# Optimization experiments

Measured on AMD Instinct MI355X. Metric: run time of the kernel, lower is better.

## Reference

```python
import jax, jax.numpy as jnp
import numpy as np

B, V, E, D_IN, D_OUT = 8, 10000, 160000, 128, 128
BN_EPS = 1e-5


def setup_inputs() -> dict:
    key = jax.random.key(0)
    ks = jax.random.split(key, 8)
    X = jax.random.normal(ks[0], (B, V, D_IN), dtype=jnp.float32)
    edge_attr = jax.random.normal(ks[1], (B, E), dtype=jnp.float32)
    W_node = jax.random.normal(ks[2], (D_OUT, D_IN), dtype=jnp.float32) * (1.0 / np.sqrt(D_IN))
    W_edge = jax.random.normal(ks[3], (D_OUT, 1), dtype=jnp.float32)
    W_self = jax.random.normal(ks[4], (D_OUT, D_IN), dtype=jnp.float32) * (1.0 / np.sqrt(D_IN))
    b_self = jax.random.normal(ks[5], (D_OUT,), dtype=jnp.float32) * 0.01
    gamma = jnp.ones((D_OUT,), dtype=jnp.float32)
    beta = jnp.zeros((D_OUT,), dtype=jnp.float32)
    edge_index = jax.random.randint(ks[6], (E, 2), 0, V, dtype=jnp.int32)
    return {"X": X, "edge_attr": edge_attr, "W_node": W_node, "W_edge": W_edge,
            "W_self": W_self, "b_self": b_self, "gamma": gamma, "beta": beta,
            "edge_index": edge_index}


def reference(X, edge_attr, W_node, W_edge, W_self, b_self, gamma, beta, edge_index):
    src = edge_index[:, 0]  # [E]
    dst = edge_index[:, 1]  # [E]
    # self-loop linear
    H = jnp.einsum('bvf,of->bvo', X, W_self) + b_self  # [B,V,D_OUT]
    # fused gather -> per-edge message -> scatter-add
    msg = jnp.einsum('bef,of->beo', X[:, src, :], W_node)  # [B,E,D_OUT]
    msg = msg + edge_attr[:, :, None] * W_edge[:, 0][None, None, :]
    aggregated = jnp.zeros_like(H).at[:, dst, :].add(msg)
    H = H + aggregated
    # BatchNorm1d over channel dim (training mode, biased variance over B*V)
    mean = jnp.mean(H, axis=(0, 1))
    var = jnp.var(H, axis=(0, 1))
    Hn = (H - mean) * jax.lax.rsqrt(var + BN_EPS) * gamma + beta
    return jax.nn.relu(Hn)
```

## Files before the change

### kernel.cpp

```cpp
#include <hip/hip_runtime.h>

#define B_ 8
#define V_ 10000
#define E_ 160000
#define DIN 128
#define DOUT 128
#define M_ (B_*V_)
#define NINV (1.0f/80000.0f)
#define BN_EPS 1e-5f

#define WS_COUNTS  0
#define WS_SUM     10000
#define WS_SUMSQ   10128
#define WS_ROWPTR  10512
#define WS_CURSOR  20513
#define WS_SSRC    30513
#define WS_SEID    190513
#define WS_S       350513
#define WS_WPK     430516
#define WS_XH      446900
#define WS_AH      5566900
#define WS_ZERO_UNITS 10256

typedef __attribute__((ext_vector_type(2))) _Float16 half2_t;
typedef __attribute__((ext_vector_type(4))) _Float16 half4_t;
typedef __attribute__((ext_vector_type(8))) _Float16 half8_t;
typedef __attribute__((ext_vector_type(4))) float f32x4;

__device__ inline half2_t i2h(unsigned i) {
    half2_t h; __builtin_memcpy(&h, &i, 4); return h;
}
__device__ inline unsigned h2i(half2_t h) {
    unsigned i; __builtin_memcpy(&i, &h, 4); return i;
}

__global__ __launch_bounds__(256) void prep_kernel(
    const float* __restrict__ X, _Float16* __restrict__ Xh,
    const float* __restrict__ Wself, const float* __restrict__ Wnode,
    _Float16* __restrict__ Wpk,
    const int* __restrict__ EI, int* __restrict__ counts)
{
    const int blk = blockIdx.x;
    const int t = threadIdx.x;
    if (blk < 10000) {
        int idx = blk * 256 + t;
        float4 v = ((const float4*)X)[idx];
        half4_t o = { (_Float16)v.x, (_Float16)v.y, (_Float16)v.z, (_Float16)v.w };
        ((half4_t*)Xh)[idx] = o;
    } else if (blk < 10016) {
        int g = (blk - 10000) * 256 + t;
        int pair = g >> 6;
        int lane = g & 63;
        int ks = pair >> 3;
        int nt = pair & 7;
        int o = nt * 16 + (lane & 15);
        int k = ks * 32 + (lane >> 4) * 8;
        const float* wsrc = (k < 128) ? (Wself + o * 128 + k)
                                      : (Wnode + o * 128 + (k - 128));
        _Float16* dst = Wpk + ((size_t)pair * 64 + lane) * 8;
#pragma unroll
        for (int j = 0; j < 8; ++j) dst[j] = (_Float16)wsrc[j];
    } else {
        int e = (blk - 10016) * 256 + t;
        if (e < E_) atomicAdd(&counts[EI[2 * e + 1]], 1);
    }
}

__global__ __launch_bounds__(256) void scan_kernel(
    const int* __restrict__ counts, int* __restrict__ row_ptr,
    int* __restrict__ cursor)
{
    __shared__ int psum[256];
    const int t = threadIdx.x;
    const int base = t * 40;
    int local[40];
    int s = 0;
#pragma unroll
    for (int i = 0; i < 40; ++i) {
        int idx = base + i;
        int c = (idx < V_) ? counts[idx] : 0;
        local[i] = s;
        s += c;
    }
    psum[t] = s;
    __syncthreads();
    for (int off = 1; off < 256; off <<= 1) {
        int v = (t >= off) ? psum[t - off] : 0;
        __syncthreads();
        psum[t] += v;
        __syncthreads();
    }
    int excl = (t == 0) ? 0 : psum[t - 1];
#pragma unroll
    for (int i = 0; i < 40; ++i) {
        int idx = base + i;
        if (idx < V_) {
            int rp = excl + local[i];
            row_ptr[idx] = rp;
            cursor[idx] = rp;
        }
    }
    if (t == 255) row_ptr[V_] = psum[255];
}

__global__ __launch_bounds__(256) void bucket_kernel(
    const int* __restrict__ EI, int* __restrict__ cursor,
    int* __restrict__ ssrc, int* __restrict__ seid)
{
    int e = blockIdx.x * 256 + threadIdx.x;
    if (e < E_) {
        int src = EI[2 * e];
        int dst = EI[2 * e + 1];
        int p = atomicAdd(&cursor[dst], 1);
        ssrc[p] = src;
        seid[p] = e;
    }
}

__global__ __launch_bounds__(256) void gather_kernel(
    const _Float16* __restrict__ Xh, const float* __restrict__ EA,
    const int* __restrict__ row_ptr, const int* __restrict__ ssrc,
    const int* __restrict__ seid, _Float16* __restrict__ Ah,
    float* __restrict__ S)
{
    const int b = blockIdx.x & 7;
    const int dblk = blockIdx.x >> 3;
    const int w = threadIdx.x >> 6;
    const int lane = threadIdx.x & 63;
    const int half = lane >> 5;
    const int sl = lane & 31;
    const int d = dblk * 4 + w;
    const int wid = b * V_ + d;
    const int k0 = row_ptr[d];
    const int k1 = row_ptr[d + 1];
    const _Float16* Xb = Xh + (size_t)b * V_ * DIN + sl * 4;
    const float* EAb = EA + (size_t)b * E_;
    half2_t a0 = (half2_t)0, a1 = (half2_t)0;
    float ea = 0.0f;
    for (int kb = k0; kb < k1; kb += 64) {
        int cnt = min(64, k1 - kb);
        int msrc = 0;
        if (lane < cnt) {
            msrc = ssrc[kb + lane];
            ea += EAb[seid[kb + lane]];
        }
        int j = 0;
        for (; j + 8 <= cnt; j += 8) {
#pragma unroll
            for (int u = 0; u < 4; ++u) {
                int s = __shfl(msrc, j + u * 2 + half);
                uint2 v = *(const uint2*)(Xb + (size_t)s * DIN);
                a0 += i2h(v.x);
                a1 += i2h(v.y);
            }
        }
        for (; j + 2 <= cnt; j += 2) {
            int s = __shfl(msrc, j + half);
            uint2 v = *(const uint2*)(Xb + (size_t)s * DIN);
            a0 += i2h(v.x);
            a1 += i2h(v.y);
        }
        if (j < cnt) {
            int s = __shfl(msrc, j);
            if (half == 0) {
                uint2 v = *(const uint2*)(Xb + (size_t)s * DIN);
                a0 += i2h(v.x);
                a1 += i2h(v.y);
            }
        }
    }
    unsigned c0 = __shfl_down(h2i(a0), 32);
    unsigned c1 = __shfl_down(h2i(a1), 32);
    a0 += i2h(c0);
    a1 += i2h(c1);
    for (int off = 32; off; off >>= 1) ea += __shfl_down(ea, off);
    if (lane == 0) S[wid] = ea;
    if (half == 0) {
        uint2 o;
        o.x = h2i(a0);
        o.y = h2i(a1);
        *(uint2*)(Ah + (size_t)wid * DIN + sl * 4) = o;
    }
}

__global__ __launch_bounds__(256) void mfma_gemm_kernel(
    const _Float16* __restrict__ Xh, const _Float16* __restrict__ Ah,
    const _Float16* __restrict__ Wpk, const float* __restrict__ S,
    const float* __restrict__ bself, const float* __restrict__ wedge,
    float* __restrict__ H, float* __restrict__ gsum, float* __restrict__ gsumsq)
{
    __shared__ float cs[128];
    __shared__ float css[128];
    const int t = threadIdx.x;
    const int wave = t >> 6;
    const int lane = t & 63;
    const int quad = lane >> 4;
    const int ln = lane & 15;
    const int rowbase = blockIdx.x * 128 + wave * 32;
    const int m0 = rowbase + ln;
    const int m1 = rowbase + 16 + ln;

    if (t < 128) { cs[t] = 0.0f; css[t] = 0.0f; }

    f32x4 acc[2][8];
#pragma unroll
    for (int mt = 0; mt < 2; ++mt)
#pragma unroll
        for (int nt = 0; nt < 8; ++nt) acc[mt][nt] = (f32x4){0.f, 0.f, 0.f, 0.f};

    const _Float16* X0 = Xh + (size_t)m0 * DIN + quad * 8;
    const _Float16* X1 = Xh + (size_t)m1 * DIN + quad * 8;
    const _Float16* A0 = Ah + (size_t)m0 * DIN + quad * 8;
    const _Float16* A1 = Ah + (size_t)m1 * DIN + quad * 8;
    const _Float16* Wl = Wpk + lane * 8;

#pragma unroll
    for (int ks = 0; ks < 8; ++ks) {
        half8_t bfr[8];
#pragma unroll
        for (int nt = 0; nt < 8; ++nt)
            bfr[nt] = *(const half8_t*)(Wl + (size_t)(ks * 8 + nt) * 512);
        half8_t af0, af1;
        if (ks < 4) {
            af0 = *(const half8_t*)(X0 + ks * 32);
            af1 = *(const half8_t*)(X1 + ks * 32);
        } else {
            af0 = *(const half8_t*)(A0 + (ks - 4) * 32);
            af1 = *(const half8_t*)(A1 + (ks - 4) * 32);
        }
#pragma unroll
        for (int nt = 0; nt < 8; ++nt) {
            acc[0][nt] = __builtin_amdgcn_mfma_f32_16x16x32_f16(af0, bfr[nt], acc[0][nt], 0, 0, 0);
            acc[1][nt] = __builtin_amdgcn_mfma_f32_16x16x32_f16(af1, bfr[nt], acc[1][nt], 0, 0, 0);
        }
    }

    float bs[8], we[8];
#pragma unroll
    for (int nt = 0; nt < 8; ++nt) {
        int c = nt * 16 + ln;
        bs[nt] = bself[c];
        we[nt] = wedge[c];
    }
    float psum[8], psq[8];
#pragma unroll
    for (int nt = 0; nt < 8; ++nt) { psum[nt] = 0.0f; psq[nt] = 0.0f; }

#pragma unroll
    for (int mt = 0; mt < 2; ++mt) {
        const int rbase = rowbase + mt * 16 + quad * 4;
        float sv[4];
#pragma unroll
        for (int r = 0; r < 4; ++r) sv[r] = S[rbase + r];
#pragma unroll
        for (int r = 0; r < 4; ++r) {
            float* Hr = H + (size_t)(rbase + r) * DOUT + ln;
#pragma unroll
            for (int nt = 0; nt < 8; ++nt) {
                float h = acc[mt][nt][r] + bs[nt] + sv[r] * we[nt];
                Hr[nt * 16] = h;
                psum[nt] += h;
                psq[nt] += h * h;
            }
        }
    }
#pragma unroll
    for (int nt = 0; nt < 8; ++nt) {
        psum[nt] += __shfl_down(psum[nt], 32);
        psum[nt] += __shfl_down(psum[nt], 16);
        psq[nt] += __shfl_down(psq[nt], 32);
        psq[nt] += __shfl_down(psq[nt], 16);
    }
    __syncthreads();
    if (lane < 16) {
#pragma unroll
        for (int nt = 0; nt < 8; ++nt) {
            atomicAdd(&cs[nt * 16 + ln], psum[nt]);
            atomicAdd(&css[nt * 16 + ln], psq[nt]);
        }
    }
    __syncthreads();
    if (t < 128) {
        atomicAdd(&gsum[t], cs[t]);
        atomicAdd(&gsumsq[t], css[t]);
    }
}

__global__ __launch_bounds__(256) void norm_relu_kernel(
    float* __restrict__ H, const float* __restrict__ gsum,
    const float* __restrict__ gsumsq, const float* __restrict__ gamma,
    const float* __restrict__ beta)
{
    int idx = blockIdx.x * 256 + threadIdx.x;
    int o4 = (idx & 31) * 4;
    float4 s = *(const float4*)(gsum + o4);
    float4 q = *(const float4*)(gsumsq + o4);
    float4 g = *(const float4*)(gamma + o4);
    float4 bt = *(const float4*)(beta + o4);
    float4 sc, sh;
    {
        float m0 = s.x * NINV, m1 = s.y * NINV, m2 = s.z * NINV, m3 = s.w * NINV;
        float r0 = rsqrtf(q.x * NINV - m0 * m0 + BN_EPS);
        float r1 = rsqrtf(q.y * NINV - m1 * m1 + BN_EPS);
        float r2 = rsqrtf(q.z * NINV - m2 * m2 + BN_EPS);
        float r3 = rsqrtf(q.w * NINV - m3 * m3 + BN_EPS);
        sc.x = g.x * r0; sc.y = g.y * r1; sc.z = g.z * r2; sc.w = g.w * r3;
        sh.x = bt.x - m0 * sc.x; sh.y = bt.y - m1 * sc.y;
        sh.z = bt.z - m2 * sc.z; sh.w = bt.w - m3 * sc.w;
    }
    float4 h = ((const float4*)H)[idx];
    h.x = fmaxf(h.x * sc.x + sh.x, 0.0f);
    h.y = fmaxf(h.y * sc.y + sh.y, 0.0f);
    h.z = fmaxf(h.z * sc.z + sh.z, 0.0f);
    h.w = fmaxf(h.w * sc.w + sh.w, 0.0f);
    ((float4*)H)[idx] = h;
}

extern "C" void kernel_launch(void* const* d_in, const int* in_sizes, int n_in,
                              void* d_out, int out_size, void* d_ws, size_t ws_size,
                              hipStream_t stream)
{
    const float* X      = (const float*)d_in[0];
    const float* EA     = (const float*)d_in[1];
    const float* Wnode  = (const float*)d_in[2];
    const float* Wedge  = (const float*)d_in[3];
    const float* Wself  = (const float*)d_in[4];
    const float* bself  = (const float*)d_in[5];
    const float* gamma  = (const float*)d_in[6];
    const float* beta   = (const float*)d_in[7];
    const int*   EI     = (const int*)d_in[8];

    int*   wsI    = (int*)d_ws;
    float* wsF    = (float*)d_ws;
    int*   counts = wsI + WS_COUNTS;
    float* gsum   = wsF + WS_SUM;
    float* gsumsq = wsF + WS_SUMSQ;
    int*   rowptr = wsI + WS_ROWPTR;
    int*   cursor = wsI + WS_CURSOR;
    int*   ssrc   = wsI + WS_SSRC;
    int*   seid   = wsI + WS_SEID;
    float* S      = wsF + WS_S;
    _Float16* Wpk = (_Float16*)(wsI + WS_WPK);
    _Float16* Xh  = (_Float16*)(wsI + WS_XH);
    _Float16* Ah  = (_Float16*)(wsI + WS_AH);
    float* H      = (float*)d_out;

    hipMemsetAsync(d_ws, 0, (size_t)WS_ZERO_UNITS * 4, stream);

    prep_kernel<<<10641, 256, 0, stream>>>(X, Xh, Wself, Wnode, Wpk, EI, counts);
    scan_kernel<<<1, 256, 0, stream>>>(counts, rowptr, cursor);
    bucket_kernel<<<(E_ + 255) / 256, 256, 0, stream>>>(EI, cursor, ssrc, seid);

    gather_kernel<<<M_ / 4, 256, 0, stream>>>(Xh, EA, rowptr, ssrc, seid, Ah, S);

    mfma_gemm_kernel<<<M_ / 128, 256, 0, stream>>>(Xh, Ah, Wpk, S, bself, Wedge,
                                                   H, gsum, gsumsq);

    norm_relu_kernel<<<(M_ * DOUT / 4) / 256, 256, 0, stream>>>(H, gsum, gsumsq,
                                                                gamma, beta);
}
```

Measured before the change: 233.3 us.

## Pre-sort edge attributes into CSR order and halve GEMM rows per block

The bucket kernel now writes all eight batch edge attributes for each edge into a CSR-ordered interleaved buffer. The gather kernel therefore reads edge attributes contiguously instead of through a random seid indirection. Separately, the MFMA GEMM now processes 16 rows per wave (64 per block) instead of 32, which doubles the grid and cuts register pressure. The trade-off is that each wave reloads the weight fragments for half as many rows, so weight reuse drops.

```diff
diff --git a/kernel.cpp b/kernel.cpp
--- a/kernel.cpp
+++ b/kernel.cpp
@@ -15,11 +15,11 @@
 #define WS_ROWPTR  10512
 #define WS_CURSOR  20513
 #define WS_SSRC    30513
-#define WS_SEID    190513
-#define WS_S       350513
-#define WS_WPK     430516
-#define WS_XH      446900
-#define WS_AH      5566900
+#define WS_EAS     190520
+#define WS_S       1470520
+#define WS_WPK     1550520
+#define WS_XH      1566904
+#define WS_AH      6686904
 #define WS_ZERO_UNITS 10256
 
 typedef __attribute__((ext_vector_type(2))) _Float16 half2_t;
@@ -104,8 +104,9 @@
 }
 
 __global__ __launch_bounds__(256) void bucket_kernel(
-    const int* __restrict__ EI, int* __restrict__ cursor,
-    int* __restrict__ ssrc, int* __restrict__ seid)
+    const int* __restrict__ EI, const float* __restrict__ EA,
+    int* __restrict__ cursor, int* __restrict__ ssrc,
+    float* __restrict__ EAs)
 {
     int e = blockIdx.x * 256 + threadIdx.x;
     if (e < E_) {
@@ -113,15 +114,20 @@
         int dst = EI[2 * e + 1];
         int p = atomicAdd(&cursor[dst], 1);
         ssrc[p] = src;
-        seid[p] = e;
+        float4 v0, v1;
+        v0.x = EA[0 * E_ + e]; v0.y = EA[1 * E_ + e];
+        v0.z = EA[2 * E_ + e]; v0.w = EA[3 * E_ + e];
+        v1.x = EA[4 * E_ + e]; v1.y = EA[5 * E_ + e];
+        v1.z = EA[6 * E_ + e]; v1.w = EA[7 * E_ + e];
+        *(float4*)(EAs + (size_t)p * 8) = v0;
+        *(float4*)(EAs + (size_t)p * 8 + 4) = v1;
     }
 }
 
 __global__ __launch_bounds__(256) void gather_kernel(
-    const _Float16* __restrict__ Xh, const float* __restrict__ EA,
+    const _Float16* __restrict__ Xh, const float* __restrict__ EAs,
     const int* __restrict__ row_ptr, const int* __restrict__ ssrc,
-    const int* __restrict__ seid, _Float16* __restrict__ Ah,
-    float* __restrict__ S)
+    _Float16* __restrict__ Ah, float* __restrict__ S)
 {
     const int b = blockIdx.x & 7;
     const int dblk = blockIdx.x >> 3;
@@ -134,7 +140,6 @@
     const int k0 = row_ptr[d];
     const int k1 = row_ptr[d + 1];
     const _Float16* Xb = Xh + (size_t)b * V_ * DIN + sl * 4;
-    const float* EAb = EA + (size_t)b * E_;
     half2_t a0 = (half2_t)0, a1 = (half2_t)0;
     float ea = 0.0f;
     for (int kb = k0; kb < k1; kb += 64) {
@@ -142,7 +147,7 @@
         int msrc = 0;
         if (lane < cnt) {
             msrc = ssrc[kb + lane];
-            ea += EAb[seid[kb + lane]];
+            ea += EAs[(size_t)(kb + lane) * 8 + b];
         }
         int j = 0;
         for (; j + 8 <= cnt; j += 8) {
@@ -196,45 +201,34 @@
     const int lane = t & 63;
     const int quad = lane >> 4;
     const int ln = lane & 15;
-    const int rowbase = blockIdx.x * 128 + wave * 32;
-    const int m0 = rowbase + ln;
-    const int m1 = rowbase + 16 + ln;
+    const int rowbase = blockIdx.x * 64 + wave * 16;
+    const int m = rowbase + ln;
 
     if (t < 128) { cs[t] = 0.0f; css[t] = 0.0f; }
 
-    f32x4 acc[2][8];
-#pragma unroll
-    for (int mt = 0; mt < 2; ++mt)
-#pragma unroll
-        for (int nt = 0; nt < 8; ++nt) acc[mt][nt] = (f32x4){0.f, 0.f, 0.f, 0.f};
-
-    const _Float16* X0 = Xh + (size_t)m0 * DIN + quad * 8;
-    const _Float16* X1 = Xh + (size_t)m1 * DIN + quad * 8;
-    const _Float16* A0 = Ah + (size_t)m0 * DIN + quad * 8;
-    const _Float16* A1 = Ah + (size_t)m1 * DIN + quad * 8;
+    f32x4 acc[8];
+#pragma unroll
+    for (int nt = 0; nt < 8; ++nt) acc[nt] = (f32x4){0.f, 0.f, 0.f, 0.f};
+
+    const _Float16* Xp = Xh + (size_t)m * DIN + quad * 8;
+    const _Float16* Ap = Ah + (size_t)m * DIN + quad * 8;
     const _Float16* Wl = Wpk + lane * 8;
 
 #pragma unroll
     for (int ks = 0; ks < 8; ++ks) {
-        half8_t bfr[8];
-#pragma unroll
-        for (int nt = 0; nt < 8; ++nt)
-            bfr[nt] = *(const half8_t*)(Wl + (size_t)(ks * 8 + nt) * 512);
-        half8_t af0, af1;
-        if (ks < 4) {
-            af0 = *(const half8_t*)(X0 + ks * 32);
-            af1 = *(const half8_t*)(X1 + ks * 32);
-        } else {
-            af0 = *(const half8_t*)(A0 + (ks - 4) * 32);
-            af1 = *(const half8_t*)(A1 + (ks - 4) * 32);
-        }
+        half8_t af = (ks < 4) ? *(const half8_t*)(Xp + ks * 32)
+                              : *(const half8_t*)(Ap + (ks - 4) * 32);
 #pragma unroll
         for (int nt = 0; nt < 8; ++nt) {
-            acc[0][nt] = __builtin_amdgcn_mfma_f32_16x16x32_f16(af0, bfr[nt], acc[0][nt], 0, 0, 0);
-            acc[1][nt] = __builtin_amdgcn_mfma_f32_16x16x32_f16(af1, bfr[nt], acc[1][nt], 0, 0, 0);
-        }
-    }
-
+            half8_t bfr = *(const half8_t*)(Wl + (size_t)(ks * 8 + nt) * 512);
+            acc[nt] = __builtin_amdgcn_mfma_f32_16x16x32_f16(af, bfr, acc[nt], 0, 0, 0);
+        }
+    }
+
+    const int rbase = rowbase + quad * 4;
+    float sv[4];
+#pragma unroll
+    for (int r = 0; r < 4; ++r) sv[r] = S[rbase + r];
     float bs[8], we[8];
 #pragma unroll
     for (int nt = 0; nt < 8; ++nt) {
@@ -245,23 +239,15 @@
     float psum[8], psq[8];
 #pragma unroll
     for (int nt = 0; nt < 8; ++nt) { psum[nt] = 0.0f; psq[nt] = 0.0f; }
-
-#pragma unroll
-    for (int mt = 0; mt < 2; ++mt) {
-        const int rbase = rowbase + mt * 16 + quad * 4;
-        float sv[4];
-#pragma unroll
-        for (int r = 0; r < 4; ++r) sv[r] = S[rbase + r];
-#pragma unroll
-        for (int r = 0; r < 4; ++r) {
-            float* Hr = H + (size_t)(rbase + r) * DOUT + ln;
-#pragma unroll
-            for (int nt = 0; nt < 8; ++nt) {
-                float h = acc[mt][nt][r] + bs[nt] + sv[r] * we[nt];
-                Hr[nt * 16] = h;
-                psum[nt] += h;
-                psq[nt] += h * h;
-            }
+#pragma unroll
+    for (int r = 0; r < 4; ++r) {
+        float* Hr = H + (size_t)(rbase + r) * DOUT + ln;
+#pragma unroll
+        for (int nt = 0; nt < 8; ++nt) {
+            float h = acc[nt][r] + bs[nt] + sv[r] * we[nt];
+            Hr[nt * 16] = h;
+            psum[nt] += h;
+            psq[nt] += h * h;
         }
     }
 #pragma unroll
@@ -338,7 +324,7 @@
     int*   rowptr = wsI + WS_ROWPTR;
     int*   cursor = wsI + WS_CURSOR;
     int*   ssrc   = wsI + WS_SSRC;
-    int*   seid   = wsI + WS_SEID;
+    float* EAs    = wsF + WS_EAS;
     float* S      = wsF + WS_S;
     _Float16* Wpk = (_Float16*)(wsI + WS_WPK);
     _Float16* Xh  = (_Float16*)(wsI + WS_XH);
@@ -349,12 +335,12 @@
 
     prep_kernel<<<10641, 256, 0, stream>>>(X, Xh, Wself, Wnode, Wpk, EI, counts);
     scan_kernel<<<1, 256, 0, stream>>>(counts, rowptr, cursor);
-    bucket_kernel<<<(E_ + 255) / 256, 256, 0, stream>>>(EI, cursor, ssrc, seid);
-
-    gather_kernel<<<M_ / 4, 256, 0, stream>>>(Xh, EA, rowptr, ssrc, seid, Ah, S);
-
-    mfma_gemm_kernel<<<M_ / 128, 256, 0, stream>>>(Xh, Ah, Wpk, S, bself, Wedge,
-                                                   H, gsum, gsumsq);
+    bucket_kernel<<<(E_ + 255) / 256, 256, 0, stream>>>(EI, EA, cursor, ssrc, EAs);
+
+    gather_kernel<<<M_ / 4, 256, 0, stream>>>(Xh, EAs, rowptr, ssrc, Ah, S);
+
+    mfma_gemm_kernel<<<M_ / 64, 256, 0, stream>>>(Xh, Ah, Wpk, S, bself, Wedge,
+                                                  H, gsum, gsumsq);
 
     norm_relu_kernel<<<(M_ * DOUT / 4) / 256, 256, 0, stream>>>(H, gsum, gsumsq,
                                                                 gamma, beta);
```

After: 240.9 us. 3.2% more time.
